# Kernel tuning notes

Hardware: AMD Instinct MI355X
Metric: run time of the kernel (lower is better)

The kernel has to match this reference:

```python
import jax, jax.numpy as jnp
import numpy as np

B, C, H, W = 4, 256, 64, 64
CS = C // 2  # in_channels // scale_factor
EPS = 1e-5


def _conv1x1(x, w, b):
    # x: [B,C,H,W], w: [O,C], b: [O]
    return jnp.einsum('bchw,oc->bohw', x, w) + b[None, :, None, None]


def setup_inputs() -> dict:
    key = jax.random.key(0)
    ks = jax.random.split(key, 12)
    sq, so = 1.0 / np.sqrt(C), 1.0 / np.sqrt(CS)
    inp = {
        'input': jax.random.normal(ks[0], (B, C, H, W), jnp.float32),
        'Wq': jax.random.normal(ks[1], (CS, C), jnp.float32) * sq,
        'bq': jax.random.normal(ks[2], (CS,), jnp.float32) * 0.01,
        'Wk': jax.random.normal(ks[3], (CS, C), jnp.float32) * sq,
        'bk': jax.random.normal(ks[4], (CS,), jnp.float32) * 0.01,
        'Wv': jax.random.normal(ks[5], (CS, C), jnp.float32) * sq,
        'bv': jax.random.normal(ks[6], (CS,), jnp.float32) * 0.01,
        'Wo': jax.random.normal(ks[7], (C, CS), jnp.float32) * so,
        'bo': jax.random.normal(ks[8], (C,), jnp.float32) * 0.01,
        'gamma': 1.0 + 0.1 * jax.random.normal(ks[9], (C,), jnp.float32),
        'beta': 0.1 * jax.random.normal(ks[10], (C,), jnp.float32),
    }
    return inp


def reference(input, Wq, bq, Wk, bk, Wv, bv, Wo, bo, gamma, beta):
    b, c, w, h = input.shape
    n = w * h
    # 1x1-conv projections -> flattened spatial tokens
    q = _conv1x1(input, Wq, bq).reshape(b, CS, n).transpose(0, 2, 1)  # [B,N,CS]
    k = _conv1x1(input, Wk, bk).reshape(b, CS, n)                     # [B,CS,N]
    attn = jax.nn.softmax(jnp.matmul(q, k), axis=-1)                  # [B,N,N]
    v = _conv1x1(input, Wv, bv).reshape(b, CS, n).transpose(0, 2, 1)  # [B,N,CS]
    out = jnp.matmul(attn, v)                                         # [B,N,CS]
    out = out.transpose(0, 2, 1).reshape(b, CS, w, h)
    # output_conv: Conv2d(1x1) -> BatchNorm2d (training-mode batch stats) -> ReLU
    y = _conv1x1(out, Wo, bo)                                         # [B,C,H,W]
    mean = y.mean(axis=(0, 2, 3))
    var = y.var(axis=(0, 2, 3))  # biased, as torch BN normalization
    yn = (y - mean[None, :, None, None]) * jax.lax.rsqrt(var + EPS)[None, :, None, None]
    yn = yn * gamma[None, :, None, None] + beta[None, :, None, None]
    return jax.nn.relu(yn) + input
```

## Files before the change

kernel.cpp:

```cpp
#include <hip/hip_runtime.h>

#define NTOK 4096
#define NCH  256
#define NCS  128
#define NBAT 4

typedef _Float16 f16;
typedef _Float16 f16x8 __attribute__((ext_vector_type(8)));
typedef _Float16 f16x4 __attribute__((ext_vector_type(4)));
typedef __fp16 fp16x2 __attribute__((ext_vector_type(2)));
typedef float f32x16 __attribute__((ext_vector_type(16)));

__device__ __forceinline__ f16 f2h(float f) { return (f16)f; }
__device__ __forceinline__ float h2f(f16 h) { return (float)h; }
__device__ __forceinline__ unsigned short h2s(f16 h) {
  union { f16 h; unsigned short s; } u; u.h = h; return u.s;
}
__device__ __forceinline__ f32x16 mfma32(f16x8 a, f16x8 b, f32x16 c) {
  return __builtin_amdgcn_mfma_f32_32x32x16_f16(a, b, c, 0, 0, 0);
}
__device__ __forceinline__ unsigned pkrtz(float a, float b) {
  union { fp16x2 h; unsigned u; } u;
  u.h = __builtin_amdgcn_cvt_pkrtz(a, b);
  return u.u;
}

__global__ void k_wconv(const float* __restrict__ wq, const float* __restrict__ wk,
                        const float* __restrict__ wv, const float* __restrict__ wo,
                        f16* __restrict__ out) {
  int i = blockIdx.x * 256 + threadIdx.x;
  int seg = i >> 15, off = i & 32767;
  const float* s = (seg == 0) ? wq : (seg == 1) ? wk : (seg == 2) ? wv : wo;
  out[i] = f2h(s[off]);
}

__launch_bounds__(768)
__global__ void k_qkv(const float* __restrict__ x,
                      const f16* __restrict__ wqb, const f16* __restrict__ wkb,
                      const f16* __restrict__ wvb,
                      const float* __restrict__ bq, const float* __restrict__ bk,
                      const float* __restrict__ bv,
                      f16* __restrict__ Qt, f16* __restrict__ Kt, f16* __restrict__ Vc) {
  __shared__ f16 Xs[32][264];
  const int tid = threadIdx.x;
  const int b = blockIdx.y;
  const int t0 = blockIdx.x * 32;
  for (int idx = tid; idx < 4096; idx += 768) {
    const int tok = idx & 31, cp = idx >> 5;
    const float* xp = x + ((size_t)(b * NCH + 2 * cp)) * NTOK + t0 + tok;
    float f0 = xp[0];
    float f1 = xp[NTOK];
    unsigned pk = (unsigned)h2s(f2h(f0)) | ((unsigned)h2s(f2h(f1)) << 16);
    *(unsigned*)&Xs[tok][2 * cp] = pk;
  }
  __syncthreads();
  const int lane = tid & 63, w = tid >> 6;
  const int p = w >> 2, nt = w & 3;
  const int cc = lane & 31, hi = lane >> 5;
  const f16* wb = (p == 0) ? wqb : (p == 1) ? wkb : wvb;
  const float* bp = (p == 0) ? bq : (p == 1) ? bk : bv;

  f32x16 acc;
  #pragma unroll
  for (int i = 0; i < 16; i++) acc[i] = 0.f;
  #pragma unroll
  for (int ks = 0; ks < 16; ks++) {
    f16x8 a = *(const f16x8*)&Xs[cc][ks * 16 + hi * 8];
    f16x8 bw = *(const f16x8*)(wb + (size_t)(nt * 32 + cc) * NCH + ks * 16 + hi * 8);
    acc = mfma32(a, bw, acc);
  }
  const int oc = nt * 32 + cc;
  const float bias = bp[oc];
  if (p < 2) {
    f16* dst = (p == 0) ? Qt : Kt;
    #pragma unroll
    for (int i = 0; i < 16; i++) {
      int row = (i & 3) + 8 * (i >> 2) + 4 * hi;
      dst[((size_t)b * NTOK + t0 + row) * NCS + oc] = f2h(acc[i] + bias);
    }
  } else {
    #pragma unroll
    for (int q = 0; q < 4; q++) {
      f16x4 pk;
      #pragma unroll
      for (int j = 0; j < 4; j++) pk[j] = f2h(acc[4 * q + j] + bias);
      *(f16x4*)(Vc + ((size_t)b * NCS + oc) * NTOK + t0 + 8 * q + 4 * hi) = pk;
    }
  }
}

__launch_bounds__(256)
__global__ void k_attn(const f16* __restrict__ Qt, const f16* __restrict__ Kt,
                       const f16* __restrict__ Vc,
                       f16* __restrict__ OP, float* __restrict__ ML, int niter) {
  __shared__ f16 Ks[64][136];
  __shared__ f16 Vs[128][72];
  __shared__ float als[4][32];
  const int tid = threadIdx.x;
  const int b = blockIdx.x & 3, kh = blockIdx.x >> 2, qt = blockIdx.y;
  const int lane = tid & 63, w = tid >> 6, cc = lane & 31, hi = lane >> 5;

  const f16* qp = Qt + ((size_t)b * NTOK + qt * 128 + w * 32 + cc) * NCS + hi * 8;
  f16x8 qf[8];
  #pragma unroll
  for (int ks = 0; ks < 8; ks++) qf[ks] = *(const f16x8*)(qp + ks * 16);

  f32x16 o[4];
  #pragma unroll
  for (int nt = 0; nt < 4; nt++)
    #pragma unroll
    for (int i = 0; i < 16; i++) o[nt][i] = 0.f;
  float m = -1e30f, l = 0.f;

  const int kkey = tid >> 2, kcb = (tid & 3) * 32;
  const int vd = tid >> 1, vh = (tid & 1) * 32;
  const int kb0 = kh * niter * 64;

  for (int it = 0; it < niter; it++) {
    const int kb = kb0 + it * 64;
    __syncthreads();
    {
      const f16* kp = Kt + ((size_t)b * NTOK + kb + kkey) * NCS + kcb;
      #pragma unroll
      for (int pp = 0; pp < 4; pp++)
        *(int4*)&Ks[kkey][kcb + pp * 8] = *(const int4*)(kp + pp * 8);
      const f16* vp = Vc + ((size_t)b * NCS + vd) * NTOK + kb + vh;
      #pragma unroll
      for (int pp = 0; pp < 4; pp++)
        *(int4*)&Vs[vd][vh + pp * 8] = *(const int4*)(vp + pp * 8);
    }
    __syncthreads();

    f32x16 s0, s1;
    #pragma unroll
    for (int i = 0; i < 16; i++) { s0[i] = 0.f; s1[i] = 0.f; }
    #pragma unroll
    for (int ks = 0; ks < 8; ks++) {
      f16x8 a0 = *(const f16x8*)&Ks[cc][ks * 16 + hi * 8];
      f16x8 a1 = *(const f16x8*)&Ks[32 + cc][ks * 16 + hi * 8];
      s0 = mfma32(a0, qf[ks], s0);
      s1 = mfma32(a1, qf[ks], s1);
    }
    float t[16];
    #pragma unroll
    for (int i = 0; i < 16; i++) t[i] = fmaxf(s0[i], s1[i]);
    #pragma unroll
    for (int st = 8; st >= 1; st >>= 1)
      #pragma unroll
      for (int i = 0; i < st; i++) t[i] = fmaxf(t[i], t[i + st]);
    const float pmax = fmaxf(t[0], __shfl_xor(t[0], 32));

    if (__all(pmax <= m)) {
      float rs = 0.f;
      #pragma unroll
      for (int i = 0; i < 16; i++) { float e = __expf(s0[i] - m); s0[i] = e; rs += e; }
      #pragma unroll
      for (int i = 0; i < 16; i++) { float e = __expf(s1[i] - m); s1[i] = e; rs += e; }
      rs += __shfl_xor(rs, 32);
      l += rs;
    } else {
      const float mnew = fmaxf(m, pmax);
      const float alpha = __expf(m - mnew);
      float rs = 0.f;
      #pragma unroll
      for (int i = 0; i < 16; i++) { float e = __expf(s0[i] - mnew); s0[i] = e; rs += e; }
      #pragma unroll
      for (int i = 0; i < 16; i++) { float e = __expf(s1[i] - mnew); s1[i] = e; rs += e; }
      rs += __shfl_xor(rs, 32);
      l = l * alpha + rs;
      m = mnew;
      if (hi == 0) als[w][cc] = alpha;
      float ar[16];
      #pragma unroll
      for (int i = 0; i < 16; i++) ar[i] = als[w][(i & 3) + 8 * (i >> 2) + 4 * hi];
      #pragma unroll
      for (int nt = 0; nt < 4; nt++)
        #pragma unroll
        for (int i = 0; i < 16; i++) o[nt][i] *= ar[i];
    }

    f16x8 pav[4];
    {
      unsigned Wt[8];
      #pragma unroll
      for (int t2 = 0; t2 < 8; t2++) Wt[t2] = pkrtz(s0[2 * t2], s0[2 * t2 + 1]);
      asm volatile("v_permlane32_swap_b32 %0, %1" : "+v"(Wt[0]), "+v"(Wt[2]));
      asm volatile("v_permlane32_swap_b32 %0, %1" : "+v"(Wt[1]), "+v"(Wt[3]));
      asm volatile("v_permlane32_swap_b32 %0, %1" : "+v"(Wt[4]), "+v"(Wt[6]));
      asm volatile("v_permlane32_swap_b32 %0, %1" : "+v"(Wt[5]), "+v"(Wt[7]));
      union { unsigned u[4]; f16x8 v; } u0, u1;
      #pragma unroll
      for (int t2 = 0; t2 < 4; t2++) { u0.u[t2] = Wt[t2]; u1.u[t2] = Wt[4 + t2]; }
      pav[0] = u0.v; pav[1] = u1.v;
      #pragma unroll
      for (int t2 = 0; t2 < 8; t2++) Wt[t2] = pkrtz(s1[2 * t2], s1[2 * t2 + 1]);
      asm volatile("v_permlane32_swap_b32 %0, %1" : "+v"(Wt[0]), "+v"(Wt[2]));
      asm volatile("v_permlane32_swap_b32 %0, %1" : "+v"(Wt[1]), "+v"(Wt[3]));
      asm volatile("v_permlane32_swap_b32 %0, %1" : "+v"(Wt[4]), "+v"(Wt[6]));
      asm volatile("v_permlane32_swap_b32 %0, %1" : "+v"(Wt[5]), "+v"(Wt[7]));
      #pragma unroll
      for (int t2 = 0; t2 < 4; t2++) { u0.u[t2] = Wt[t2]; u1.u[t2] = Wt[4 + t2]; }
      pav[2] = u0.v; pav[3] = u1.v;
    }

    #pragma unroll
    for (int ks = 0; ks < 4; ks++) {
      #pragma unroll
      for (int nt = 0; nt < 4; nt++) {
        f16x8 bv = *(const f16x8*)&Vs[nt * 32 + cc][ks * 16 + hi * 8];
        o[nt] = mfma32(pav[ks], bv, o[nt]);
      }
    }
  }
  const size_t obase = (((size_t)kh * NBAT + b) * NTOK + qt * 128 + w * 32);
  if (hi == 0) {
    const size_t mi = obase + cc;
    ML[mi * 2] = m; ML[mi * 2 + 1] = l;
  }
  #pragma unroll
  for (int nt = 0; nt < 4; nt++)
    #pragma unroll
    for (int i = 0; i < 16; i++) {
      int row = (i & 3) + 8 * (i >> 2) + 4 * hi;
      OP[(obase + row) * NCS + nt * 32 + cc] = f2h(o[nt][i]);
    }
}

template <int S>
__global__ void k_comb(const f16* __restrict__ OP, const float* __restrict__ ML,
                       f16* __restrict__ Oa) {
  const int gid = blockIdx.x * 256 + threadIdx.x;
  const int tok = gid >> 4, dg = (gid & 15) * 8;
  const int b = tok >> 12, tn = tok & 4095;
  float mv[S], lv[S];
  float mm = -1e30f;
  #pragma unroll
  for (int s = 0; s < S; s++) {
    const size_t idx = (((size_t)s * NBAT + b) * NTOK + tn);
    mv[s] = ML[idx * 2]; lv[s] = ML[idx * 2 + 1];
    mm = fmaxf(mm, mv[s]);
  }
  float den = 0.f, wsc[S];
  #pragma unroll
  for (int s = 0; s < S; s++) { wsc[s] = __expf(mv[s] - mm); den += wsc[s] * lv[s]; }
  const float inv = 1.f / den;
  float oacc[8];
  #pragma unroll
  for (int j = 0; j < 8; j++) oacc[j] = 0.f;
  #pragma unroll
  for (int s = 0; s < S; s++) {
    const size_t idx = (((size_t)s * NBAT + b) * NTOK + tn);
    int4 v = *(const int4*)(OP + idx * NCS + dg);
    const f16* a = (const f16*)&v;
    #pragma unroll
    for (int j = 0; j < 8; j++) oacc[j] += wsc[s] * h2f(a[j]);
  }
  f16x8 vv;
  #pragma unroll
  for (int j = 0; j < 8; j++) vv[j] = f2h(oacc[j] * inv);
  *(f16x8*)(Oa + ((size_t)b * NTOK + tn) * NCS + dg) = vv;
}

__launch_bounds__(256)
__global__ void k_out(const f16* __restrict__ Oa, const f16* __restrict__ wob,
                      const float* __restrict__ bo,
                      f16* __restrict__ Yb, float* __restrict__ Psum) {
  __shared__ f16 Es[256][72];
  const int tid = threadIdx.x;
  const int b = blockIdx.y, tt = blockIdx.x, t0 = tt * 64;
  const int lane = tid & 63, w = tid >> 6, cc = lane & 31, hi = lane >> 5;
  const int th = w >> 1, oh = w & 1;
  const f16* op = Oa + ((size_t)b * NTOK + t0 + th * 32 + cc) * NCS + hi * 8;
  f16x8 af[8];
  #pragma unroll
  for (int ks = 0; ks < 8; ks++) af[ks] = *(const f16x8*)(op + ks * 16);
  f32x16 acc[4];
  #pragma unroll
  for (int nt = 0; nt < 4; nt++)
    #pragma unroll
    for (int i = 0; i < 16; i++) acc[nt][i] = 0.f;
  #pragma unroll
  for (int ks = 0; ks < 8; ks++)
    #pragma unroll
    for (int nt = 0; nt < 4; nt++) {
      f16x8 bw = *(const f16x8*)(wob + (size_t)(oh * 128 + nt * 32 + cc) * NCS + ks * 16 + hi * 8);
      acc[nt] = mfma32(af[ks], bw, acc[nt]);
    }
  #pragma unroll
  for (int nt = 0; nt < 4; nt++) {
    const int co = oh * 128 + nt * 32 + cc;
    const float bias = bo[co];
    float s = 0.f, sq = 0.f;
    #pragma unroll
    for (int i = 0; i < 16; i++) {
      float v = acc[nt][i] + bias;
      acc[nt][i] = v; s += v; sq += v * v;
    }
    s += __shfl_xor(s, 32); sq += __shfl_xor(sq, 32);
    if (hi == 0) {
      const size_t pi = ((size_t)(b * 64 + tt) * 2 + th) * NCH + co;
      Psum[pi * 2] = s; Psum[pi * 2 + 1] = sq;
    }
    #pragma unroll
    for (int q = 0; q < 4; q++) {
      f16x4 pk;
      #pragma unroll
      for (int j = 0; j < 4; j++) pk[j] = f2h(acc[nt][4 * q + j]);
      *(f16x4*)&Es[co][th * 32 + q * 8 + hi * 4] = pk;
    }
  }
  __syncthreads();
  {
    const f16* er = &Es[tid][0];
    f16* yp = Yb + ((size_t)b * NCH + tid) * NTOK + t0;
    #pragma unroll
    for (int p = 0; p < 8; p++)
      *(int4*)(yp + p * 8) = *(const int4*)(er + p * 8);
  }
}

__global__ void k_stats(const float* __restrict__ Psum, float* __restrict__ St) {
  const int ch = blockIdx.x, tid = threadIdx.x;
  float s = 0.f, sq = 0.f;
  for (int i = tid; i < 512; i += 128) {
    s  += Psum[((size_t)i * NCH + ch) * 2];
    sq += Psum[((size_t)i * NCH + ch) * 2 + 1];
  }
  #pragma unroll
  for (int off = 32; off >= 1; off >>= 1) { s += __shfl_down(s, off); sq += __shfl_down(sq, off); }
  __shared__ float red[4];
  if ((tid & 63) == 0) { red[(tid >> 6) * 2] = s; red[(tid >> 6) * 2 + 1] = sq; }
  __syncthreads();
  if (tid == 0) {
    s = red[0] + red[2]; sq = red[1] + red[3];
    const float mean = s * (1.f / 16384.f);
    const float var = sq * (1.f / 16384.f) - mean * mean;
    St[ch * 2] = mean;
    St[ch * 2 + 1] = 1.f / sqrtf(var + 1e-5f);
  }
}

__global__ void k_final(const f16* __restrict__ Yb, const float* __restrict__ x,
                        const float* __restrict__ St, const float* __restrict__ gamma,
                        const float* __restrict__ beta, float* __restrict__ out) {
  const size_t i = ((size_t)blockIdx.x * 256 + threadIdx.x) * 8;
  const int ch = (int)((i >> 12) & 255);
  const float mean = St[ch * 2], rstd = St[ch * 2 + 1];
  const float sc = gamma[ch] * rstd;
  const float sh = beta[ch] - mean * sc;
  int4 yv = *(const int4*)(Yb + i);
  const f16* ys = (const f16*)&yv;
  const float4 x0 = *(const float4*)(x + i);
  const float4 x1 = *(const float4*)(x + i + 4);
  float4 o0, o1;
  o0.x = fmaxf(h2f(ys[0]) * sc + sh, 0.f) + x0.x;
  o0.y = fmaxf(h2f(ys[1]) * sc + sh, 0.f) + x0.y;
  o0.z = fmaxf(h2f(ys[2]) * sc + sh, 0.f) + x0.z;
  o0.w = fmaxf(h2f(ys[3]) * sc + sh, 0.f) + x0.w;
  o1.x = fmaxf(h2f(ys[4]) * sc + sh, 0.f) + x1.x;
  o1.y = fmaxf(h2f(ys[5]) * sc + sh, 0.f) + x1.y;
  o1.z = fmaxf(h2f(ys[6]) * sc + sh, 0.f) + x1.z;
  o1.w = fmaxf(h2f(ys[7]) * sc + sh, 0.f) + x1.w;
  *(float4*)(out + i) = o0;
  *(float4*)(out + i + 4) = o1;
}

extern "C" void kernel_launch(void* const* d_in, const int* in_sizes, int n_in,
                              void* d_out, int out_size, void* d_ws, size_t ws_size,
                              hipStream_t stream) {
  const float* x     = (const float*)d_in[0];
  const float* Wq    = (const float*)d_in[1];
  const float* bq    = (const float*)d_in[2];
  const float* Wk    = (const float*)d_in[3];
  const float* bk    = (const float*)d_in[4];
  const float* Wv    = (const float*)d_in[5];
  const float* bv    = (const float*)d_in[6];
  const float* Wo    = (const float*)d_in[7];
  const float* bo    = (const float*)d_in[8];
  const float* gamma = (const float*)d_in[9];
  const float* beta  = (const float*)d_in[10];
  float* out = (float*)d_out;
  char* ws = (char*)d_ws;

  const size_t OFF_W  = 0;
  const size_t OFF_QT = 262144;
  const size_t OFF_KT = OFF_QT + 4194304;
  const size_t OFF_VC = OFF_KT + 4194304;
  const size_t OFF_OP = OFF_VC + 4194304;
  const size_t opsz8 = (size_t)8 * NBAT * NTOK * NCS * 2;
  const size_t mlsz8 = (size_t)8 * NBAT * NTOK * 2 * 4;
  const size_t need8 = OFF_OP + opsz8 + mlsz8 + 1048576 + 4096;
  const int SPLIT = (ws_size >= need8) ? 8 : 4;
  const size_t opsz = (size_t)SPLIT * NBAT * NTOK * NCS * 2;
  const size_t mlsz = (size_t)SPLIT * NBAT * NTOK * 2 * 4;
  const size_t OFF_ML = OFF_OP + opsz;
  const size_t OFF_PS = OFF_ML + mlsz;
  const size_t OFF_ST = OFF_PS + 1048576;

  f16* wqb = (f16*)(ws + OFF_W);
  f16* wkb = (f16*)(ws + OFF_W + 65536);
  f16* wvb = (f16*)(ws + OFF_W + 131072);
  f16* wob = (f16*)(ws + OFF_W + 196608);
  f16* Qt  = (f16*)(ws + OFF_QT);
  f16* Kt  = (f16*)(ws + OFF_KT);
  f16* Vc  = (f16*)(ws + OFF_VC);
  f16* OP  = (f16*)(ws + OFF_OP);
  float* ML = (float*)(ws + OFF_ML);
  float* Psum = (float*)(ws + OFF_PS);
  float* St   = (float*)(ws + OFF_ST);
  f16* Yb = (f16*)(ws + OFF_QT);
  f16* Oa = (f16*)(ws + OFF_VC);

  k_wconv<<<512, 256, 0, stream>>>(Wq, Wk, Wv, Wo, wqb);
  k_qkv<<<dim3(128, 4), 768, 0, stream>>>(x, wqb, wkb, wvb, bq, bk, bv, Qt, Kt, Vc);
  k_attn<<<dim3(4 * SPLIT, 32), 256, 0, stream>>>(Qt, Kt, Vc, OP, ML, 64 / SPLIT);
  if (SPLIT == 8) k_comb<8><<<1024, 256, 0, stream>>>(OP, ML, Oa);
  else            k_comb<4><<<1024, 256, 0, stream>>>(OP, ML, Oa);
  k_out<<<dim3(64, 4), 256, 0, stream>>>(Oa, wob, bo, Yb, Psum);
  k_stats<<<256, 128, 0, stream>>>(Psum, St);
  k_final<<<2048, 256, 0, stream>>>(Yb, x, St, gamma, beta, out);
}
```

Baseline: 217.9 us.

## Double-buffer K/V tiles in attention kernel with register prefetch

The attention kernel now keeps two LDS buffers for the K and V tiles. Each iteration issues global loads for the next tile into registers before the QK and PV MFMA work, then writes them to the other buffer afterwards, leaving one barrier per iteration instead of two. The aim is to hide global load latency behind the matrix math. In exchange it doubles LDS use, keeps eight int4 registers live across the compute, and adds a launch-bounds hint for two blocks per CU that may cap register allocation.

```diff
diff --git a/kernel.cpp b/kernel.cpp
--- a/kernel.cpp
+++ b/kernel.cpp
@@ -89,12 +89,12 @@
   }
 }
 
-__launch_bounds__(256)
+__launch_bounds__(256, 2)
 __global__ void k_attn(const f16* __restrict__ Qt, const f16* __restrict__ Kt,
                        const f16* __restrict__ Vc,
                        f16* __restrict__ OP, float* __restrict__ ML, int niter) {
-  __shared__ f16 Ks[64][136];
-  __shared__ f16 Vs[128][72];
+  __shared__ f16 Ks[2][64][136];
+  __shared__ f16 Vs[2][128][72];
   __shared__ float als[4][32];
   const int tid = threadIdx.x;
   const int b = blockIdx.x & 3, kh = blockIdx.x >> 2, qt = blockIdx.y;
@@ -115,29 +115,41 @@
   const int kkey = tid >> 2, kcb = (tid & 3) * 32;
   const int vd = tid >> 1, vh = (tid & 1) * 32;
   const int kb0 = kh * niter * 64;
+  const f16* kbase = Kt + ((size_t)b * NTOK + kkey) * NCS + kcb;
+  const f16* vbase = Vc + ((size_t)b * NCS + vd) * NTOK + vh;
+
+  {
+    const f16* kp = kbase + (size_t)kb0 * NCS;
+    const f16* vp = vbase + kb0;
+    #pragma unroll
+    for (int pp = 0; pp < 4; pp++) {
+      *(int4*)&Ks[0][kkey][kcb + pp * 8] = *(const int4*)(kp + pp * 8);
+      *(int4*)&Vs[0][vd][vh + pp * 8] = *(const int4*)(vp + pp * 8);
+    }
+  }
+  __syncthreads();
 
   for (int it = 0; it < niter; it++) {
-    const int kb = kb0 + it * 64;
-    __syncthreads();
-    {
-      const f16* kp = Kt + ((size_t)b * NTOK + kb + kkey) * NCS + kcb;
-      #pragma unroll
-      for (int pp = 0; pp < 4; pp++)
-        *(int4*)&Ks[kkey][kcb + pp * 8] = *(const int4*)(kp + pp * 8);
-      const f16* vp = Vc + ((size_t)b * NCS + vd) * NTOK + kb + vh;
-      #pragma unroll
-      for (int pp = 0; pp < 4; pp++)
-        *(int4*)&Vs[vd][vh + pp * 8] = *(const int4*)(vp + pp * 8);
-    }
-    __syncthreads();
+    const int cur = it & 1;
+    int4 kr0, kr1, kr2, kr3, vr0, vr1, vr2, vr3;
+    const bool pf = (it + 1 < niter);
+    if (pf) {
+      const int kb = kb0 + (it + 1) * 64;
+      const f16* kp = kbase + (size_t)kb * NCS;
+      const f16* vp = vbase + kb;
+      kr0 = *(const int4*)(kp);      kr1 = *(const int4*)(kp + 8);
+      kr2 = *(const int4*)(kp + 16); kr3 = *(const int4*)(kp + 24);
+      vr0 = *(const int4*)(vp);      vr1 = *(const int4*)(vp + 8);
+      vr2 = *(const int4*)(vp + 16); vr3 = *(const int4*)(vp + 24);
+    }
 
     f32x16 s0, s1;
     #pragma unroll
     for (int i = 0; i < 16; i++) { s0[i] = 0.f; s1[i] = 0.f; }
     #pragma unroll
     for (int ks = 0; ks < 8; ks++) {
-      f16x8 a0 = *(const f16x8*)&Ks[cc][ks * 16 + hi * 8];
-      f16x8 a1 = *(const f16x8*)&Ks[32 + cc][ks * 16 + hi * 8];
+      f16x8 a0 = *(const f16x8*)&Ks[cur][cc][ks * 16 + hi * 8];
+      f16x8 a1 = *(const f16x8*)&Ks[cur][32 + cc][ks * 16 + hi * 8];
       s0 = mfma32(a0, qf[ks], s0);
       s1 = mfma32(a1, qf[ks], s1);
     }
@@ -207,10 +219,23 @@
     for (int ks = 0; ks < 4; ks++) {
       #pragma unroll
       for (int nt = 0; nt < 4; nt++) {
-        f16x8 bv = *(const f16x8*)&Vs[nt * 32 + cc][ks * 16 + hi * 8];
+        f16x8 bv = *(const f16x8*)&Vs[cur][nt * 32 + cc][ks * 16 + hi * 8];
         o[nt] = mfma32(pav[ks], bv, o[nt]);
       }
     }
+
+    if (pf) {
+      const int nxt = cur ^ 1;
+      *(int4*)&Ks[nxt][kkey][kcb]      = kr0;
+      *(int4*)&Ks[nxt][kkey][kcb + 8]  = kr1;
+      *(int4*)&Ks[nxt][kkey][kcb + 16] = kr2;
+      *(int4*)&Ks[nxt][kkey][kcb + 24] = kr3;
+      *(int4*)&Vs[nxt][vd][vh]      = vr0;
+      *(int4*)&Vs[nxt][vd][vh + 8]  = vr1;
+      *(int4*)&Vs[nxt][vd][vh + 16] = vr2;
+      *(int4*)&Vs[nxt][vd][vh + 24] = vr3;
+    }
+    __syncthreads();
   }
   const size_t obase = (((size_t)kh * NBAT + b) * NTOK + qt * 128 + w * 32);
   if (hi == 0) {
```

New measurement: 207.1 us. 5.0% less time.
